# Kernel optimization log

Measured on AMD Instinct MI355X. Metric: run time of the kernel, lower is better.

The kernel has to match this reference:

```python
import jax, jax.numpy as jnp
import numpy as np

N_NODES = 20000
N_EDGES = 320000
F_IN = 256
HID = 256
N_CLS = 5


def _glorot(key, shape):
    lim = np.sqrt(6.0 / (shape[0] + shape[1]))
    return jax.random.uniform(key, shape, jnp.float32, -lim, lim)


def setup_inputs() -> dict:
    key = jax.random.key(0)
    ks = jax.random.split(key, 12)
    x1 = jax.random.normal(ks[0], (N_NODES, F_IN), jnp.float32)
    x2 = jax.random.normal(ks[1], (N_NODES, F_IN), jnp.float32)
    ei1 = jax.random.randint(ks[2], (2, N_EDGES), 0, N_NODES, jnp.int64 if jax.config.jax_enable_x64 else jnp.int32)
    ei2 = jax.random.randint(ks[3], (2, N_EDGES), 0, N_NODES, jnp.int64 if jax.config.jax_enable_x64 else jnp.int32)
    params = {
        'W1': _glorot(ks[4], (F_IN, HID)), 'b1': jnp.zeros((HID,), jnp.float32),
        'W2': _glorot(ks[5], (HID, HID)), 'b2': jnp.zeros((HID,), jnp.float32),
        'W3': _glorot(ks[6], (HID, HID)), 'b3': jnp.zeros((HID,), jnp.float32),
        'Wl': _glorot(ks[7], (HID, N_CLS)), 'bl': jnp.zeros((N_CLS,), jnp.float32),
    }
    return {'x1': x1, 'edge_index1': ei1, 'x2': x2, 'edge_index2': ei2, **params}


def gcn_conv(x, edge_index, W, b):
    # PyG GCNConv: add self-loops, symmetric normalization D^-1/2 (A+I) D^-1/2 (X W) + b
    N = x.shape[0]
    src, dst = edge_index[0], edge_index[1]
    deg = jax.ops.segment_sum(jnp.ones(src.shape[0], x.dtype), dst, num_segments=N) + 1.0
    dinv = jax.lax.rsqrt(deg)  # [N]
    xw = x @ W                 # [N, H]
    coef = (dinv[src] * dinv[dst])[:, None]  # per-edge norm
    agg = jax.ops.segment_sum(xw[src] * coef, dst, num_segments=N)
    agg = agg + xw * (dinv * dinv)[:, None]  # self-loop term
    return agg + b


def _branch(x, ei, W1, b1, W2, b2, W3, b3):
    # dropout is identity in eval mode
    h = jax.nn.relu(gcn_conv(x, ei, W1, b1))
    h = jax.nn.relu(gcn_conv(h, ei, W2, b2))
    return gcn_conv(h, ei, W3, b3)


def reference(x1, edge_index1, x2, edge_index2, W1, b1, W2, b2, W3, b3, Wl, bl):
    h1 = _branch(x1, edge_index1, W1, b1, W2, b2, W3, b3)
    h2 = _branch(x2, edge_index2, W1, b1, W2, b2, W3, b3)
    h = jnp.concatenate([h1, h2], axis=0)          # [2N, H]
    pooled = jnp.mean(h, axis=0, keepdims=True)    # batch is all zeros -> single mean pool
    return pooled @ Wl + bl                        # [1, num_classes]
```

## Files before the change

kernel.cpp:

```cpp
#include <hip/hip_runtime.h>
#include <hip/hip_bf16.h>

#define N_NODES 20000
#define N_EDGES 320000
#define HID 256
#define NQ 5000
#define NCHUNK 64

typedef __attribute__((ext_vector_type(8))) short bf16x8;
typedef __attribute__((ext_vector_type(4))) float f32x4;
typedef __attribute__((ext_vector_type(8))) unsigned short us8;

__device__ __forceinline__ float bf2f(ushort u) {
  union { unsigned int i; float f; } v; v.i = ((unsigned int)u) << 16; return v.f;
}
__device__ __forceinline__ ushort f2bf(float f) {
  union { float f; unsigned int i; } v; v.f = f;
  unsigned int r = v.i + 0x7FFFu + ((v.i >> 16) & 1u);
  return (ushort)(r >> 16);
}

__global__ void init_detect_kernel(int* cnt0, int* cnt1, float* t0, float* t1,
                                   const void* x1, const void* ei1, int* flags) {
  if (blockIdx.x == gridDim.x - 1) {
    __shared__ int cnt_wild, cnt_oddnz;
    if (threadIdx.x == 0) { cnt_wild = 0; cnt_oddnz = 0; }
    __syncthreads();
    const ushort* xu = (const ushort*)x1;
    int wild = 0;
#pragma unroll
    for (int k = 0; k < 4; k++) {
      ushort u = xu[threadIdx.x * 4 + k];
      int ex = (u >> 7) & 0xFF;
      if (ex >= 0x90) wild++;
    }
    if (wild) atomicAdd(&cnt_wild, wild);
    const int* ii = (const int*)ei1;
    if (ii[threadIdx.x * 2 + 1] != 0) atomicAdd(&cnt_oddnz, 1);
    __syncthreads();
    if (threadIdx.x == 0) {
      flags[0] = (cnt_wild > 64) ? 1 : 0;
      flags[1] = (cnt_oddnz < 8) ? 1 : 0;
    }
    return;
  }
  int i = blockIdx.x * blockDim.x + threadIdx.x;
  if (i < N_NODES) { cnt0[i] = 0; cnt1[i] = 0; t0[i] = 0.f; t1[i] = 0.f; }
}

__global__ __launch_bounds__(256) void wt_kernel(
    const void* __restrict__ W1, const void* __restrict__ W2,
    ushort* __restrict__ Wt1, ushort* __restrict__ Wt2,
    const int* __restrict__ flags) {
  bool f32 = flags[0] != 0;
  int which = blockIdx.x >> 8;
  int k = blockIdx.x & 255;
  const void* W = which ? W2 : W1;
  ushort* Wt = which ? Wt2 : Wt1;
  int n = threadIdx.x;
  ushort v = f32 ? f2bf(((const float*)W)[k * 256 + n])
                 : ((const ushort*)W)[k * 256 + n];
  Wt[n * 256 + k] = v;
}

__global__ __launch_bounds__(1024) void count_rank_kernel(
    const void* e0, const void* e1, int* cnt0, int* cnt1,
    int* rank0, int* rank1, const int* flags) {
  int b = blockIdx.y;
  const void* e = b ? e1 : e0;
  int* cnt = b ? cnt1 : cnt0;
  int* rank = b ? rank1 : rank0;
  int chunk = blockIdx.x >> 2;
  int lo = (blockIdx.x & 3) * NQ;
  int ebeg = chunk * (N_EDGES / NCHUNK);
  int eend = ebeg + (N_EDGES / NCHUNK);
  __shared__ int hist[NQ];
  __shared__ int base[NQ];
  for (int k = threadIdx.x; k < NQ; k += 1024) hist[k] = 0;
  __syncthreads();
  bool w64 = flags[1] != 0;
  const int* d32 = (const int*)e + N_EDGES;
  const long long* d64 = (const long long*)e + N_EDGES;
  for (int i = ebeg + threadIdx.x; i < eend; i += 1024) {
    int d = w64 ? (int)d64[i] : d32[i];
    unsigned q = (unsigned)(d - lo);
    if (q < NQ) atomicAdd(&hist[q], 1);
  }
  __syncthreads();
  for (int k = threadIdx.x; k < NQ; k += 1024) {
    int h = hist[k];
    if (h) base[k] = atomicAdd(&cnt[lo + k], h);
    hist[k] = 0;
  }
  __syncthreads();
  for (int i = ebeg + threadIdx.x; i < eend; i += 1024) {
    int d = w64 ? (int)d64[i] : d32[i];
    unsigned q = (unsigned)(d - lo);
    if (q < NQ) rank[i] = base[q] + atomicAdd(&hist[q], 1);
  }
}

__global__ __launch_bounds__(1024) void scan_kernel(const int* cnt0, const int* cnt1,
                                                    int* rp0, int* rp1,
                                                    float* dinv0, float* dinv1) {
  const int* cnt = blockIdx.x ? cnt1 : cnt0;
  int* rp = blockIdx.x ? rp1 : rp0;
  float* dinv = blockIdx.x ? dinv1 : dinv0;
  __shared__ int sd[1024];
  int tid = threadIdx.x;
  int base = tid * 20;
  int pref[20];
  int run = 0;
#pragma unroll
  for (int k = 0; k < 20; k++) {
    int i = base + k;
    int c = (i < N_NODES) ? cnt[i] : 0;
    if (i < N_NODES) dinv[i] = rsqrtf((float)c + 1.0f);
    run += c;
    pref[k] = run;
  }
  sd[tid] = run;
  __syncthreads();
  for (int off = 1; off < 1024; off <<= 1) {
    int v = (tid >= off) ? sd[tid - off] : 0;
    __syncthreads();
    sd[tid] += v;
    __syncthreads();
  }
  int offset = sd[tid] - run;
  if (tid == 0) rp[0] = 0;
#pragma unroll
  for (int k = 0; k < 20; k++) {
    int i = base + k;
    if (i < N_NODES) rp[i + 1] = offset + pref[k];
  }
}

__global__ __launch_bounds__(1024) void fill_kernel(
    const void* e0, const void* e1,
    const float* dinv0, const float* dinv1,
    const int* rp0, const int* rp1,
    const int* rank0, const int* rank1,
    unsigned int* eg0, unsigned int* eg1,
    float* t0, float* t1, const int* flags) {
  int b = blockIdx.y;
  const void* e = b ? e1 : e0;
  const float* dinv = b ? dinv1 : dinv0;
  bool w64 = flags[1] != 0;
  const int* s32 = (const int*)e;
  const int* d32 = (const int*)e + N_EDGES;
  const long long* s64 = (const long long*)e;
  const long long* d64 = (const long long*)e + N_EDGES;
  if (blockIdx.x < 313) {
    const int* rp = b ? rp1 : rp0;
    const int* rank = b ? rank1 : rank0;
    unsigned int* eg = b ? eg1 : eg0;
    int i = blockIdx.x * 1024 + threadIdx.x;
    if (i >= N_EDGES) return;
    int src = w64 ? (int)s64[i] : s32[i];
    int dst = w64 ? (int)d64[i] : d32[i];
    int slot = rp[dst] + rank[i];
    eg[slot] = (unsigned int)src | ((unsigned int)f2bf(dinv[src] * dinv[dst]) << 16);
    return;
  }
  float* t = b ? t1 : t0;
  int r = blockIdx.x - 313;
  int chunk = r >> 2;
  int lo = (r & 3) * NQ;
  int ebeg = chunk * (N_EDGES / NCHUNK);
  int eend = ebeg + (N_EDGES / NCHUNK);
  __shared__ float tl[NQ];
  for (int k = threadIdx.x; k < NQ; k += 1024) tl[k] = 0.f;
  __syncthreads();
  for (int i = ebeg + threadIdx.x; i < eend; i += 1024) {
    int src = w64 ? (int)s64[i] : s32[i];
    unsigned q = (unsigned)(src - lo);
    if (q < NQ) {
      int dst = w64 ? (int)d64[i] : d32[i];
      atomicAdd(&tl[q], dinv[dst]);
    }
  }
  __syncthreads();
  for (int k = threadIdx.x; k < NQ; k += 1024) {
    float v = tl[k];
    if (v != 0.f) atomicAdd(&t[lo + k], v);
  }
}

__global__ __launch_bounds__(256) void gemm_kernel(
    const void* __restrict__ A0, const void* __restrict__ A1,
    const ushort* __restrict__ Wt,
    ushort* __restrict__ C0, ushort* __restrict__ C1,
    int maybe_f32, const int* __restrict__ flags) {
  const void* A = blockIdx.z ? A1 : A0;
  ushort* C = blockIdx.z ? C1 : C0;
  bool af32 = maybe_f32 && (flags[0] != 0);
  int m0 = blockIdx.x * 32;
  __shared__ __align__(16) ushort As[32][264];
  int tid = threadIdx.x;
  int wave = tid >> 6, lane = tid & 63;
  int quad = lane >> 4, r16 = lane & 15;
  int nb = wave * 64;
  {
    int row = tid >> 3, c0 = (tid & 7) * 32;
    int gr = m0 + row;
    if (af32) {
      const float* pA = (const float*)A + gr * 256 + c0;
      ushort* d = &As[row][c0];
#pragma unroll
      for (int s = 0; s < 8; s++) {
        float4 v = *(const float4*)(pA + s * 4);
        d[s * 4 + 0] = f2bf(v.x); d[s * 4 + 1] = f2bf(v.y);
        d[s * 4 + 2] = f2bf(v.z); d[s * 4 + 3] = f2bf(v.w);
      }
    } else {
      const ushort* pA = (const ushort*)A + gr * 256 + c0;
#pragma unroll
      for (int s = 0; s < 4; s++)
        *(int4*)&As[row][c0 + s * 8] = *(const int4*)(pA + s * 8);
    }
  }
  __syncthreads();
  f32x4 acc[2][4];
#pragma unroll
  for (int m = 0; m < 2; m++)
#pragma unroll
    for (int n = 0; n < 4; n++) acc[m][n] = (f32x4){0.f, 0.f, 0.f, 0.f};
#pragma unroll
  for (int k0 = 0; k0 < 256; k0 += 32) {
    bf16x8 a0 = *(const bf16x8*)&As[r16][k0 + quad * 8];
    bf16x8 a1 = *(const bf16x8*)&As[16 + r16][k0 + quad * 8];
    const ushort* wp = Wt + (nb + r16) * 256 + k0 + quad * 8;
    bf16x8 bb0 = *(const bf16x8*)(wp);
    bf16x8 bb1 = *(const bf16x8*)(wp + 16 * 256);
    bf16x8 bb2 = *(const bf16x8*)(wp + 32 * 256);
    bf16x8 bb3 = *(const bf16x8*)(wp + 48 * 256);
    acc[0][0] = __builtin_amdgcn_mfma_f32_16x16x32_bf16(a0, bb0, acc[0][0], 0, 0, 0);
    acc[0][1] = __builtin_amdgcn_mfma_f32_16x16x32_bf16(a0, bb1, acc[0][1], 0, 0, 0);
    acc[0][2] = __builtin_amdgcn_mfma_f32_16x16x32_bf16(a0, bb2, acc[0][2], 0, 0, 0);
    acc[0][3] = __builtin_amdgcn_mfma_f32_16x16x32_bf16(a0, bb3, acc[0][3], 0, 0, 0);
    acc[1][0] = __builtin_amdgcn_mfma_f32_16x16x32_bf16(a1, bb0, acc[1][0], 0, 0, 0);
    acc[1][1] = __builtin_amdgcn_mfma_f32_16x16x32_bf16(a1, bb1, acc[1][1], 0, 0, 0);
    acc[1][2] = __builtin_amdgcn_mfma_f32_16x16x32_bf16(a1, bb2, acc[1][2], 0, 0, 0);
    acc[1][3] = __builtin_amdgcn_mfma_f32_16x16x32_bf16(a1, bb3, acc[1][3], 0, 0, 0);
  }
#pragma unroll
  for (int m = 0; m < 2; m++) {
    int grb = m0 + m * 16 + quad * 4;
#pragma unroll
    for (int r = 0; r < 4; r++) {
      int gr = grb + r;
      ushort* cp = C + gr * 256 + nb + r16;
      cp[0]  = f2bf(acc[m][0][r]);
      cp[16] = f2bf(acc[m][1][r]);
      cp[32] = f2bf(acc[m][2][r]);
      cp[48] = f2bf(acc[m][3][r]);
    }
  }
}

__global__ __launch_bounds__(256) void agg_kernel(
    const ushort* __restrict__ XW0, const ushort* __restrict__ XW1,
    const float* __restrict__ dinv0, const float* __restrict__ dinv1,
    const int* __restrict__ rp0, const int* __restrict__ rp1,
    const unsigned int* __restrict__ eg0, const unsigned int* __restrict__ eg1,
    const void* __restrict__ bias,
    ushort* __restrict__ H0, ushort* __restrict__ H1,
    const int* __restrict__ flags) {
  int b = blockIdx.y;
  const ushort* XW = b ? XW1 : XW0;
  const float* dinv = b ? dinv1 : dinv0;
  const int* rp = b ? rp1 : rp0;
  const unsigned int* eg = b ? eg1 : eg0;
  ushort* H = b ? H1 : H0;
  int wave = threadIdx.x >> 6, lane = threadIdx.x & 63;
  int grp = lane >> 3;
  int fo = (lane & 7) * 8 + blockIdx.z * 64;
  int i = blockIdx.x * 32 + wave * 8 + grp;
  float di = dinv[i];
  float selfw = di * di;
  us8 v = *(const us8*)(XW + i * 256 + fo);
  float acc[8], acc2[8];
#pragma unroll
  for (int k = 0; k < 8; k++) { acc[k] = selfw * bf2f(v[k]); acc2[k] = 0.f; }
  int e = rp[i], eend = rp[i + 1];
  for (; e + 4 <= eend; e += 4) {
    unsigned int p0 = eg[e], p1 = eg[e + 1], p2 = eg[e + 2], p3 = eg[e + 3];
    us8 r0 = *(const us8*)(XW + (p0 & 0xFFFFu) * 256 + fo);
    us8 r1 = *(const us8*)(XW + (p1 & 0xFFFFu) * 256 + fo);
    us8 r2 = *(const us8*)(XW + (p2 & 0xFFFFu) * 256 + fo);
    us8 r3 = *(const us8*)(XW + (p3 & 0xFFFFu) * 256 + fo);
    float w0 = bf2f((ushort)(p0 >> 16)), w1 = bf2f((ushort)(p1 >> 16));
    float w2 = bf2f((ushort)(p2 >> 16)), w3 = bf2f((ushort)(p3 >> 16));
#pragma unroll
    for (int k = 0; k < 8; k++) {
      acc[k]  += w0 * bf2f(r0[k]);
      acc2[k] += w1 * bf2f(r1[k]);
      acc[k]  += w2 * bf2f(r2[k]);
      acc2[k] += w3 * bf2f(r3[k]);
    }
  }
  for (; e < eend; e++) {
    unsigned int pp = eg[e];
    us8 r = *(const us8*)(XW + (pp & 0xFFFFu) * 256 + fo);
    float w = bf2f((ushort)(pp >> 16));
#pragma unroll
    for (int k = 0; k < 8; k++) acc[k] += w * bf2f(r[k]);
  }
  float bv[8];
  if (flags[0]) {
    const float* bf = (const float*)bias + fo;
    float4 c0 = *(const float4*)bf;
    float4 c1 = *(const float4*)(bf + 4);
    bv[0] = c0.x; bv[1] = c0.y; bv[2] = c0.z; bv[3] = c0.w;
    bv[4] = c1.x; bv[5] = c1.y; bv[6] = c1.z; bv[7] = c1.w;
  } else {
    us8 bb = *(const us8*)((const ushort*)bias + fo);
#pragma unroll
    for (int k = 0; k < 8; k++) bv[k] = bf2f(bb[k]);
  }
  us8 o;
#pragma unroll
  for (int k = 0; k < 8; k++)
    o[k] = f2bf(fmaxf(acc[k] + acc2[k] + bv[k], 0.f));
  *(us8*)(H + i * 256 + fo) = o;
}

__global__ __launch_bounds__(256) void colsum_kernel(
    const ushort* __restrict__ H0, const ushort* __restrict__ H1,
    const float* __restrict__ dinv0, const float* __restrict__ dinv1,
    const float* __restrict__ t0, const float* __restrict__ t1,
    float* __restrict__ P) {
  int b = blockIdx.y;
  const ushort* H = b ? H1 : H0;
  const float* dinv = b ? dinv1 : dinv0;
  const float* t = b ? t1 : t0;
  int wave = threadIdx.x >> 6, lane = threadIdx.x & 63;
  int wid = blockIdx.x * 4 + wave;
  int f4 = lane * 4;
  float a0 = 0.f, a1 = 0.f, a2 = 0.f, a3 = 0.f;
  for (int j = wid; j < N_NODES; j += 256) {
    float dj = dinv[j];
    float c = dj * (t[j] + dj);
    ushort4 u = *(const ushort4*)(H + j * 256 + f4);
    a0 += c * bf2f(u.x); a1 += c * bf2f(u.y);
    a2 += c * bf2f(u.z); a3 += c * bf2f(u.w);
  }
  __shared__ float part[4][256];
  part[wave][f4 + 0] = a0; part[wave][f4 + 1] = a1;
  part[wave][f4 + 2] = a2; part[wave][f4 + 3] = a3;
  __syncthreads();
  int f = threadIdx.x;
  float ssum = part[0][f] + part[1][f] + part[2][f] + part[3][f];
  P[(b * 64 + blockIdx.x) * 256 + f] = ssum;
}

__global__ __launch_bounds__(256) void final_kernel(
    const float* __restrict__ P,
    const void* __restrict__ W3, const void* __restrict__ b3,
    const void* __restrict__ Wl, const void* __restrict__ bl,
    void* __restrict__ out, const int* __restrict__ flags) {
  __shared__ float v[256];
  __shared__ float pooled[256];
  bool f32 = flags[0] != 0;
  int t = threadIdx.x;
  float acc0 = 0.f, acc1 = 0.f;
  for (int b = 0; b < 64; b++) {
    acc0 += P[b * 256 + t];
    acc1 += P[(64 + b) * 256 + t];
  }
  v[t] = acc0 + acc1;
  __syncthreads();
  float acc = 0.f;
  if (f32) {
    const float* W3f = (const float*)W3;
    for (int f = 0; f < 256; f++) acc += v[f] * W3f[f * 256 + t];
    pooled[t] = acc * (1.0f / (2.0f * N_NODES)) + ((const float*)b3)[t];
  } else {
    const ushort* W3b = (const ushort*)W3;
    for (int f = 0; f < 256; f++) acc += v[f] * bf2f(W3b[f * 256 + t]);
    pooled[t] = acc * (1.0f / (2.0f * N_NODES)) + bf2f(((const ushort*)b3)[t]);
  }
  __syncthreads();
  if (t < 5) {
    float o;
    if (f32) {
      o = ((const float*)bl)[t];
      for (int h = 0; h < 256; h++) o += pooled[h] * ((const float*)Wl)[h * 5 + t];
      ((float*)out)[t] = o;
    } else {
      o = bf2f(((const ushort*)bl)[t]);
      for (int h = 0; h < 256; h++) o += pooled[h] * bf2f(((const ushort*)Wl)[h * 5 + t]);
      ((ushort*)out)[t] = f2bf(o);
    }
  }
}

extern "C" void kernel_launch(void* const* d_in, const int* in_sizes, int n_in,
                              void* d_out, int out_size, void* d_ws, size_t ws_size,
                              hipStream_t stream) {
  const void* x1 = d_in[0];
  const void* ei1 = d_in[1];
  const void* x2 = d_in[2];
  const void* ei2 = d_in[3];
  const void* W1 = d_in[4];
  const void* b1 = d_in[5];
  const void* W2 = d_in[6];
  const void* b2 = d_in[7];
  const void* W3 = d_in[8];
  const void* b3 = d_in[9];
  const void* Wl = d_in[10];
  const void* bl = d_in[11];

  char* p = (char*)d_ws;
  auto alloc = [&](size_t bytes) {
    char* r = p;
    p += (bytes + 255) & ~size_t(255);
    return r;
  };
  int* flags   = (int*)alloc(256);
  float* dinv0 = (float*)alloc(N_NODES * 4);
  float* dinv1 = (float*)alloc(N_NODES * 4);
  float* t0    = (float*)alloc(N_NODES * 4);
  float* t1    = (float*)alloc(N_NODES * 4);
  int* cnt0    = (int*)alloc(N_NODES * 4);
  int* cnt1    = (int*)alloc(N_NODES * 4);
  int* rp0     = (int*)alloc((N_NODES + 1) * 4);
  int* rp1     = (int*)alloc((N_NODES + 1) * 4);
  unsigned int* eg0 = (unsigned int*)alloc((size_t)N_EDGES * 4);
  unsigned int* eg1 = (unsigned int*)alloc((size_t)N_EDGES * 4);
  float* Pp    = (float*)alloc(2 * 64 * 256 * 4);
  ushort* wt1  = (ushort*)alloc(256 * 256 * 2);
  ushort* wt2  = (ushort*)alloc(256 * 256 * 2);
  ushort* xw0  = (ushort*)alloc((size_t)N_NODES * HID * 2);
  ushort* xw1  = (ushort*)alloc((size_t)N_NODES * HID * 2);
  ushort* h0   = (ushort*)alloc((size_t)N_NODES * HID * 2);
  ushort* h1   = (ushort*)alloc((size_t)N_NODES * HID * 2);
  int* rank0  = (int*)xw0;
  int* rank1  = rank0 + N_EDGES;

  init_detect_kernel<<<(N_NODES + 255) / 256 + 1, 256, 0, stream>>>(
      cnt0, cnt1, t0, t1, x1, ei1, flags);
  wt_kernel<<<512, 256, 0, stream>>>(W1, W2, wt1, wt2, flags);
  count_rank_kernel<<<dim3(NCHUNK * 4, 2), 1024, 0, stream>>>(
      ei1, ei2, cnt0, cnt1, rank0, rank1, flags);
  scan_kernel<<<2, 1024, 0, stream>>>(cnt0, cnt1, rp0, rp1, dinv0, dinv1);
  fill_kernel<<<dim3(313 + NCHUNK * 4, 2), 1024, 0, stream>>>(
      ei1, ei2, dinv0, dinv1, rp0, rp1, rank0, rank1, eg0, eg1, t0, t1, flags);

  gemm_kernel<<<dim3(625, 1, 2), 256, 0, stream>>>(x1, x2, wt1, xw0, xw1, 1, flags);
  agg_kernel<<<dim3(625, 2, 4), 256, 0, stream>>>(
      xw0, xw1, dinv0, dinv1, rp0, rp1, eg0, eg1, b1, h0, h1, flags);

  gemm_kernel<<<dim3(625, 1, 2), 256, 0, stream>>>(h0, h1, wt2, xw0, xw1, 0, flags);
  agg_kernel<<<dim3(625, 2, 4), 256, 0, stream>>>(
      xw0, xw1, dinv0, dinv1, rp0, rp1, eg0, eg1, b2, h0, h1, flags);

  colsum_kernel<<<dim3(64, 2), 256, 0, stream>>>(h0, h1, dinv0, dinv1, t0, t1, Pp);
  final_kernel<<<1, 256, 0, stream>>>(Pp, W3, b3, Wl, bl, d_out, flags);
}
```

Before: 353.8 us.

## Fuse weighted column-sum into second aggregation and shrink setup block sizes

The second aggregation pass now folds its ReLU output into a per-block weighted column sum held in shared memory and adds it atomically into a 512-float accumulator. This replaces the separate colsum kernel and avoids writing and re-reading the second hidden layer. Block sizes for the count/rank and fill kernels also drop from 1024 to 512 threads. The trade-off is many shared and global float atomics, which make the summation order nondeterministic and may contend.

```diff
diff --git a/kernel.cpp b/kernel.cpp
--- a/kernel.cpp
+++ b/kernel.cpp
@@ -21,6 +21,7 @@
 }
 
 __global__ void init_detect_kernel(int* cnt0, int* cnt1, float* t0, float* t1,
+                                   float* P,
                                    const void* x1, const void* ei1, int* flags) {
   if (blockIdx.x == gridDim.x - 1) {
     __shared__ int cnt_wild, cnt_oddnz;
@@ -46,6 +47,7 @@
   }
   int i = blockIdx.x * blockDim.x + threadIdx.x;
   if (i < N_NODES) { cnt0[i] = 0; cnt1[i] = 0; t0[i] = 0.f; t1[i] = 0.f; }
+  if (i < 512) P[i] = 0.f;
 }
 
 __global__ __launch_bounds__(256) void wt_kernel(
@@ -63,7 +65,7 @@
   Wt[n * 256 + k] = v;
 }
 
-__global__ __launch_bounds__(1024) void count_rank_kernel(
+__global__ __launch_bounds__(512) void count_rank_kernel(
     const void* e0, const void* e1, int* cnt0, int* cnt1,
     int* rank0, int* rank1, const int* flags) {
   int b = blockIdx.y;
@@ -76,24 +78,24 @@
   int eend = ebeg + (N_EDGES / NCHUNK);
   __shared__ int hist[NQ];
   __shared__ int base[NQ];
-  for (int k = threadIdx.x; k < NQ; k += 1024) hist[k] = 0;
+  for (int k = threadIdx.x; k < NQ; k += 512) hist[k] = 0;
   __syncthreads();
   bool w64 = flags[1] != 0;
   const int* d32 = (const int*)e + N_EDGES;
   const long long* d64 = (const long long*)e + N_EDGES;
-  for (int i = ebeg + threadIdx.x; i < eend; i += 1024) {
+  for (int i = ebeg + threadIdx.x; i < eend; i += 512) {
     int d = w64 ? (int)d64[i] : d32[i];
     unsigned q = (unsigned)(d - lo);
     if (q < NQ) atomicAdd(&hist[q], 1);
   }
   __syncthreads();
-  for (int k = threadIdx.x; k < NQ; k += 1024) {
+  for (int k = threadIdx.x; k < NQ; k += 512) {
     int h = hist[k];
     if (h) base[k] = atomicAdd(&cnt[lo + k], h);
     hist[k] = 0;
   }
   __syncthreads();
-  for (int i = ebeg + threadIdx.x; i < eend; i += 1024) {
+  for (int i = ebeg + threadIdx.x; i < eend; i += 512) {
     int d = w64 ? (int)d64[i] : d32[i];
     unsigned q = (unsigned)(d - lo);
     if (q < NQ) rank[i] = base[q] + atomicAdd(&hist[q], 1);
@@ -136,7 +138,7 @@
   }
 }
 
-__global__ __launch_bounds__(1024) void fill_kernel(
+__global__ __launch_bounds__(512) void fill_kernel(
     const void* e0, const void* e1,
     const float* dinv0, const float* dinv1,
     const int* rp0, const int* rp1,
@@ -151,12 +153,11 @@
   const int* d32 = (const int*)e + N_EDGES;
   const long long* s64 = (const long long*)e;
   const long long* d64 = (const long long*)e + N_EDGES;
-  if (blockIdx.x < 313) {
+  if (blockIdx.x < 625) {
     const int* rp = b ? rp1 : rp0;
     const int* rank = b ? rank1 : rank0;
     unsigned int* eg = b ? eg1 : eg0;
-    int i = blockIdx.x * 1024 + threadIdx.x;
-    if (i >= N_EDGES) return;
+    int i = blockIdx.x * 512 + threadIdx.x;
     int src = w64 ? (int)s64[i] : s32[i];
     int dst = w64 ? (int)d64[i] : d32[i];
     int slot = rp[dst] + rank[i];
@@ -164,15 +165,15 @@
     return;
   }
   float* t = b ? t1 : t0;
-  int r = blockIdx.x - 313;
+  int r = blockIdx.x - 625;
   int chunk = r >> 2;
   int lo = (r & 3) * NQ;
   int ebeg = chunk * (N_EDGES / NCHUNK);
   int eend = ebeg + (N_EDGES / NCHUNK);
   __shared__ float tl[NQ];
-  for (int k = threadIdx.x; k < NQ; k += 1024) tl[k] = 0.f;
-  __syncthreads();
-  for (int i = ebeg + threadIdx.x; i < eend; i += 1024) {
+  for (int k = threadIdx.x; k < NQ; k += 512) tl[k] = 0.f;
+  __syncthreads();
+  for (int i = ebeg + threadIdx.x; i < eend; i += 512) {
     int src = w64 ? (int)s64[i] : s32[i];
     unsigned q = (unsigned)(src - lo);
     if (q < NQ) {
@@ -181,7 +182,7 @@
     }
   }
   __syncthreads();
-  for (int k = threadIdx.x; k < NQ; k += 1024) {
+  for (int k = threadIdx.x; k < NQ; k += 512) {
     float v = tl[k];
     if (v != 0.f) atomicAdd(&t[lo + k], v);
   }
@@ -266,13 +267,18 @@
     const unsigned int* __restrict__ eg0, const unsigned int* __restrict__ eg1,
     const void* __restrict__ bias,
     ushort* __restrict__ H0, ushort* __restrict__ H1,
+    const float* __restrict__ t0, const float* __restrict__ t1,
+    float* __restrict__ Pacc, int fuse,
     const int* __restrict__ flags) {
+  __shared__ float ps[64];
   int b = blockIdx.y;
   const ushort* XW = b ? XW1 : XW0;
   const float* dinv = b ? dinv1 : dinv0;
   const int* rp = b ? rp1 : rp0;
   const unsigned int* eg = b ? eg1 : eg0;
   ushort* H = b ? H1 : H0;
+  if (threadIdx.x < 64) ps[threadIdx.x] = 0.f;
+  __syncthreads();
   int wave = threadIdx.x >> 6, lane = threadIdx.x & 63;
   int grp = lane >> 3;
   int fo = (lane & 7) * 8 + blockIdx.z * 64;
@@ -319,40 +325,25 @@
 #pragma unroll
     for (int k = 0; k < 8; k++) bv[k] = bf2f(bb[k]);
   }
-  us8 o;
-#pragma unroll
-  for (int k = 0; k < 8; k++)
-    o[k] = f2bf(fmaxf(acc[k] + acc2[k] + bv[k], 0.f));
-  *(us8*)(H + i * 256 + fo) = o;
-}
-
-__global__ __launch_bounds__(256) void colsum_kernel(
-    const ushort* __restrict__ H0, const ushort* __restrict__ H1,
-    const float* __restrict__ dinv0, const float* __restrict__ dinv1,
-    const float* __restrict__ t0, const float* __restrict__ t1,
-    float* __restrict__ P) {
-  int b = blockIdx.y;
-  const ushort* H = b ? H1 : H0;
-  const float* dinv = b ? dinv1 : dinv0;
-  const float* t = b ? t1 : t0;
-  int wave = threadIdx.x >> 6, lane = threadIdx.x & 63;
-  int wid = blockIdx.x * 4 + wave;
-  int f4 = lane * 4;
-  float a0 = 0.f, a1 = 0.f, a2 = 0.f, a3 = 0.f;
-  for (int j = wid; j < N_NODES; j += 256) {
-    float dj = dinv[j];
-    float c = dj * (t[j] + dj);
-    ushort4 u = *(const ushort4*)(H + j * 256 + f4);
-    a0 += c * bf2f(u.x); a1 += c * bf2f(u.y);
-    a2 += c * bf2f(u.z); a3 += c * bf2f(u.w);
-  }
-  __shared__ float part[4][256];
-  part[wave][f4 + 0] = a0; part[wave][f4 + 1] = a1;
-  part[wave][f4 + 2] = a2; part[wave][f4 + 3] = a3;
-  __syncthreads();
-  int f = threadIdx.x;
-  float ssum = part[0][f] + part[1][f] + part[2][f] + part[3][f];
-  P[(b * 64 + blockIdx.x) * 256 + f] = ssum;
+  if (fuse) {
+    float ti = (b ? t1 : t0)[i];
+    float ci = di * (ti + di);
+    int fl = (lane & 7) * 8;
+#pragma unroll
+    for (int k = 0; k < 8; k++) {
+      float hv = fmaxf(acc[k] + acc2[k] + bv[k], 0.f);
+      atomicAdd(&ps[fl + k], ci * hv);
+    }
+  } else {
+    us8 o;
+#pragma unroll
+    for (int k = 0; k < 8; k++)
+      o[k] = f2bf(fmaxf(acc[k] + acc2[k] + bv[k], 0.f));
+    *(us8*)(H + i * 256 + fo) = o;
+  }
+  __syncthreads();
+  if (fuse && threadIdx.x < 64)
+    atomicAdd(&Pacc[b * 256 + blockIdx.z * 64 + threadIdx.x], ps[threadIdx.x]);
 }
 
 __global__ __launch_bounds__(256) void final_kernel(
@@ -364,12 +355,7 @@
   __shared__ float pooled[256];
   bool f32 = flags[0] != 0;
   int t = threadIdx.x;
-  float acc0 = 0.f, acc1 = 0.f;
-  for (int b = 0; b < 64; b++) {
-    acc0 += P[b * 256 + t];
-    acc1 += P[(64 + b) * 256 + t];
-  }
-  v[t] = acc0 + acc1;
+  v[t] = P[t] + P[256 + t];
   __syncthreads();
   float acc = 0.f;
   if (f32) {
@@ -429,7 +415,7 @@
   int* rp1     = (int*)alloc((N_NODES + 1) * 4);
   unsigned int* eg0 = (unsigned int*)alloc((size_t)N_EDGES * 4);
   unsigned int* eg1 = (unsigned int*)alloc((size_t)N_EDGES * 4);
-  float* Pp    = (float*)alloc(2 * 64 * 256 * 4);
+  float* Pp    = (float*)alloc(512 * 4);
   ushort* wt1  = (ushort*)alloc(256 * 256 * 2);
   ushort* wt2  = (ushort*)alloc(256 * 256 * 2);
   ushort* xw0  = (ushort*)alloc((size_t)N_NODES * HID * 2);
@@ -440,22 +426,23 @@
   int* rank1  = rank0 + N_EDGES;
 
   init_detect_kernel<<<(N_NODES + 255) / 256 + 1, 256, 0, stream>>>(
-      cnt0, cnt1, t0, t1, x1, ei1, flags);
+      cnt0, cnt1, t0, t1, Pp, x1, ei1, flags);
   wt_kernel<<<512, 256, 0, stream>>>(W1, W2, wt1, wt2, flags);
-  count_rank_kernel<<<dim3(NCHUNK * 4, 2), 1024, 0, stream>>>(
+  count_rank_kernel<<<dim3(NCHUNK * 4, 2), 512, 0, stream>>>(
       ei1, ei2, cnt0, cnt1, rank0, rank1, flags);
   scan_kernel<<<2, 1024, 0, stream>>>(cnt0, cnt1, rp0, rp1, dinv0, dinv1);
-  fill_kernel<<<dim3(313 + NCHUNK * 4, 2), 1024, 0, stream>>>(
+  fill_kernel<<<dim3(625 + NCHUNK * 4, 2), 512, 0, stream>>>(
       ei1, ei2, dinv0, dinv1, rp0, rp1, rank0, rank1, eg0, eg1, t0, t1, flags);
 
   gemm_kernel<<<dim3(625, 1, 2), 256, 0, stream>>>(x1, x2, wt1, xw0, xw1, 1, flags);
   agg_kernel<<<dim3(625, 2, 4), 256, 0, stream>>>(
-      xw0, xw1, dinv0, dinv1, rp0, rp1, eg0, eg1, b1, h0, h1, flags);
+      xw0, xw1, dinv0, dinv1, rp0, rp1, eg0, eg1, b1, h0, h1,
+      t0, t1, Pp, 0, flags);
 
   gemm_kernel<<<dim3(625, 1, 2), 256, 0, stream>>>(h0, h1, wt2, xw0, xw1, 0, flags);
   agg_kernel<<<dim3(625, 2, 4), 256, 0, stream>>>(
-      xw0, xw1, dinv0, dinv1, rp0, rp1, eg0, eg1, b2, h0, h1, flags);
-
-  colsum_kernel<<<dim3(64, 2), 256, 0, stream>>>(h0, h1, dinv0, dinv1, t0, t1, Pp);
+      xw0, xw1, dinv0, dinv1, rp0, rp1, eg0, eg1, b2, h0, h1,
+      t0, t1, Pp, 1, flags);
+
   final_kernel<<<1, 256, 0, stream>>>(Pp, W3, b3, Wl, bl, d_out, flags);
 }
```

Result: slower. 402.5 us (+13.8%).
